# Kernel optimization log

Measured on AMD Instinct MI355X. Metric: run time of the kernel, lower is better.

## Reference

```python
import jax, jax.numpy as jnp
import numpy as np

# Config matching init_kwargs / input shapes
DIM = 96        # dim == C
NH = 6          # num_heads
KS = 7          # kernel_size (local window)
GW = 4          # group_width for the grouped conv in Hadamard-attn branch
B, D, H, W = 2, 8, 96, 96
HD = DIM // NH          # head dim (dim_qk == dim_v == dim)
SCALE = HD ** -0.5      # qk_scale default: head_dim**-0.5
PAD = KS // 2
EPS = 1e-5


def setup_inputs() -> dict:
    key = jax.random.key(0)
    ks = jax.random.split(key, 10)
    s = 0.02
    return {
        "x": jax.random.normal(ks[0], (B, DIM, D, H, W), jnp.float32),
        # pre-norm LayerNorm params
        "ln_g": jnp.ones((DIM,), jnp.float32),
        "ln_b": jnp.zeros((DIM,), jnp.float32),
        # q,k projection (fused 1x1): out = 2*dim_qk
        "w_qk": s * jax.random.normal(ks[1], (2 * DIM, DIM), jnp.float32),
        "b_qk": jnp.zeros((2 * DIM,), jnp.float32),
        # v projection (1x1)
        "w_v": s * jax.random.normal(ks[2], (DIM, DIM), jnp.float32),
        "b_v": jnp.zeros((DIM,), jnp.float32),
        # Hadamard-attention branch: grouped KSxKS conv (groups = DIM//GW)
        "w_a1": s * jax.random.normal(ks[3], (DIM, GW, KS, KS), jnp.float32),
        "b_a1": jnp.zeros((DIM,), jnp.float32),
        # 1x1 conv producing per-head local attention logits (NH * KS^2 channels)
        "w_a2": s * jax.random.normal(ks[4], (NH * KS * KS, DIM), jnp.float32),
        "b_a2": jnp.zeros((NH * KS * KS,), jnp.float32),
        # ghost head (lam=1, gamma=1): attn = h_attn * ghost_mul + ghost_add
        "g_mul": 1.0 + s * jax.random.normal(ks[5], (NH * KS * KS,), jnp.float32),
        "g_add": s * jax.random.normal(ks[6], (NH * KS * KS,), jnp.float32),
        # output projection (1x1)
        "w_p": s * jax.random.normal(ks[7], (DIM, DIM), jnp.float32),
        "b_p": jnp.zeros((DIM,), jnp.float32),
    }


def _elsa_block(x, ln_g, ln_b, w_qk, b_qk, w_v, b_v, w_a1, b_a1, w_a2, b_a2,
                g_mul, g_add, w_p, b_p):
    """x: (Bp, H, W, C) channel-last frames. Pre-norm residual ELSA attention."""
    Bp, Hh, Ww, C = x.shape
    # LayerNorm over channels
    mu = jnp.mean(x, axis=-1, keepdims=True)
    var = jnp.mean(jnp.square(x - mu), axis=-1, keepdims=True)
    xn = (x - mu) * jax.lax.rsqrt(var + EPS) * ln_g + ln_b

    # 1x1 q,k,v projections (channel-last matmuls)
    qk = xn @ w_qk.T + b_qk                      # (Bp,H,W,2C)
    q, k = jnp.split(qk, 2, axis=-1)
    v = xn @ w_v.T + b_v                         # (Bp,H,W,C)

    # Hadamard product -> attention logits via grouped conv + GELU + 1x1
    h = jnp.transpose(q * k * SCALE, (0, 3, 1, 2))   # (Bp,C,H,W) NCHW
    a = jax.lax.conv_general_dilated(
        h, w_a1, window_strides=(1, 1), padding='SAME',
        feature_group_count=C // GW) + b_a1[None, :, None, None]
    a = jax.nn.gelu(a, approximate=False)
    a = jnp.einsum('bchw,oc->bohw', a, w_a2) + b_a2[None, :, None, None]

    # ghost head (lam=1, gamma=1): elementwise scale + static bias per (head, tap)
    attn = a * g_mul[None, :, None, None] + g_add[None, :, None, None]
    attn = attn.reshape(Bp, NH, KS * KS, Hh, Ww)     # (Bp,nh,k^2,H,W)

    # local window aggregation (unfold-free: 49 shifted fused multiply-adds)
    vr = jnp.transpose(v, (0, 3, 1, 2)).reshape(Bp, NH, HD, Hh, Ww)
    vp = jnp.pad(vr, ((0, 0), (0, 0), (0, 0), (PAD, PAD), (PAD, PAD)))
    out = jnp.zeros_like(vr)
    for i in range(KS):
        for j in range(KS):
            out = out + attn[:, :, i * KS + j, None] * vp[:, :, :, i:i + Hh, j:j + Ww]

    out = jnp.transpose(out.reshape(Bp, C, Hh, Ww), (0, 2, 3, 1))  # (Bp,H,W,C)
    y = out @ w_p.T + b_p
    return x + y


def reference(x, ln_g, ln_b, w_qk, b_qk, w_v, b_v, w_a1, b_a1, w_a2, b_a2,
              g_mul, g_add, w_p, b_p):
    b, c, d, hh, ww = x.shape
    # 'b c s h w -> (b s) h w c'
    xf = jnp.transpose(x, (0, 2, 3, 4, 1)).reshape(b * d, hh, ww, c)
    yf = _elsa_block(xf, ln_g, ln_b, w_qk, b_qk, w_v, b_v, w_a1, b_a1,
                     w_a2, b_a2, g_mul, g_add, w_p, b_p)
    # '(b s) h w c -> b c s h w'
    return jnp.transpose(yf.reshape(b, d, hh, ww, c), (0, 4, 1, 2, 3))
```

## Files before the change

### kernel.cpp

```cpp
#include <hip/hip_runtime.h>
#include <hip/hip_bf16.h>


typedef unsigned short u16;
typedef short bf16x8 __attribute__((ext_vector_type(8)));
typedef float floatx4 __attribute__((ext_vector_type(4)));
typedef unsigned short ushort8 __attribute__((ext_vector_type(8)));
typedef unsigned short ushort4v __attribute__((ext_vector_type(4)));
typedef unsigned int uint4v __attribute__((ext_vector_type(4)));
typedef unsigned int uint2v __attribute__((ext_vector_type(2)));

#define PIX      9216
#define SCALE_QK 0.25f

__device__ __forceinline__ float b2f(u16 u) {
  union { unsigned int i; float f; } z; z.i = ((unsigned int)u) << 16; return z.f;
}
__device__ __forceinline__ float lo2f(unsigned int u) {
  union { unsigned int i; float f; } z; z.i = u << 16; return z.f;
}
__device__ __forceinline__ float hi2f(unsigned int u) {
  union { unsigned int i; float f; } z; z.i = u & 0xFFFF0000u; return z.f;
}
__device__ __forceinline__ u16 f2b(float f) {
  union { float f; unsigned int i; } z; z.f = f;
  unsigned int r = z.i + 0x7fffu + ((z.i >> 16) & 1u);
  return (u16)(r >> 16);
}

__global__ void k_prep(const float* __restrict__ w_qk, const float* __restrict__ b_qk,
                       const float* __restrict__ w_v,  const float* __restrict__ b_v,
                       const float* __restrict__ w_a1,
                       const float* __restrict__ w_a2, const float* __restrict__ b_a2,
                       const float* __restrict__ g_mul,const float* __restrict__ g_add,
                       const float* __restrict__ w_p,  const float* __restrict__ b_p,
                       u16* __restrict__ W2, float* __restrict__ bias2,
                       u16* __restrict__ WA2, float* __restrict__ biasA2,
                       u16* __restrict__ WP, float* __restrict__ biasP,
                       float* __restrict__ WC1) {
  int i = blockIdx.x * 256 + threadIdx.x;
  if (i < 30720) {
    int r = i / 96, ci = i % 96;
    float val = 0.f;
    if (r < 192) { int src = (r & 1) ? (96 + (r >> 1)) : (r >> 1); val = w_qk[src * 96 + ci]; }
    else if (r < 288) val = w_v[(r - 192) * 96 + ci];
    W2[i] = f2b(val);
  } else if (i < 31040) {
    int r = i - 30720; float bv = 0.f;
    if (r < 192) { int src = (r & 1) ? (96 + (r >> 1)) : (r >> 1); bv = b_qk[src]; }
    else if (r < 288) bv = b_v[r - 192];
    bias2[r] = bv;
  } else if (i < 61760) {
    int j = i - 31040; int r = j / 96, ci = j % 96;
    float wv = 0.f;
    if (r < 294) wv = w_a2[r * 96 + ci] * g_mul[r];
    WA2[j] = f2b(wv);
  } else if (i < 62080) {
    int r = i - 61760; float bv = 0.f;
    if (r < 294) bv = b_a2[r] * g_mul[r] + g_add[r];
    biasA2[r] = bv;
  } else if (i < 74368) {
    int j = i - 62080; int r = j / 96;
    WP[j] = (r < 96) ? f2b(w_p[j]) : (u16)0;
  } else if (i < 74496) {
    int r = i - 74368;
    biasP[r] = (r < 96) ? b_p[r] : 0.f;
  } else if (i < 93312) {
    int j = i - 74496;
    int co = j & 3, kx = (j >> 2) % 7, ky = (j / 28) % 7, ch = (j / 196) & 3, g = j / 784;
    WC1[j] = w_a1[(g * 4 + co) * 196 + ch * 49 + ky * 7 + kx];
  }
}

__global__ __launch_bounds__(256) void k_ln(const float* __restrict__ x,
                                            const float* __restrict__ lg,
                                            const float* __restrict__ lb,
                                            u16* __restrict__ xn) {
  int idx = blockIdx.x * 256 + threadIdx.x;
  int f = idx / PIX, p = idx % PIX;
  int b = f >> 3, d = f & 7;
  size_t base = ((size_t)(b * 768 + d)) * PIX + p;
  float s = 0.f, ss = 0.f;
  for (int c = 0; c < 96; ++c) {
    float v = x[base + (size_t)c * 73728];
    s += v; ss += v * v;
  }
  float mu = s * (1.f / 96.f);
  float var = ss * (1.f / 96.f) - mu * mu;
  float rs = rsqrtf(var + 1e-5f);
  size_t ob = (size_t)idx * 96;
  for (int c0 = 0; c0 < 96; c0 += 8) {
    ushort8 pack;
    for (int u = 0; u < 8; ++u) {
      int c = c0 + u;
      float v = x[base + (size_t)c * 73728];
      pack[u] = f2b((v - mu) * rs * lg[c] + lb[c]);
    }
    *(ushort8*)&xn[ob + c0] = pack;
  }
}

template <int MODE>
__global__ __launch_bounds__(256) void k_gemm(const u16* __restrict__ X,
                                              const u16* __restrict__ W,
                                              const float* __restrict__ bias,
                                              u16* __restrict__ out0,
                                              u16* __restrict__ out1,
                                              float* __restrict__ outF,
                                              const float* __restrict__ resid,
                                              int fArg) {
  __shared__ u16 lw[64 * 104];
  __shared__ u16 lx[64 * 104];
  const int tid = threadIdx.x;
  const int fc = blockIdx.z;
  const int f = (MODE == 1) ? (fArg + fc) : fc;
  const int p0 = blockIdx.x * 64;
  const int cot = blockIdx.y;

  if constexpr (MODE == 0) {
    for (int ch = tid; ch < 768; ch += 256) {
      int r = ch / 12, s2 = ch % 12;
      *(uint4v*)&lw[r * 104 + s2 * 8] = *(const uint4v*)&W[(size_t)(cot * 64 + r) * 96 + s2 * 8];
      *(uint4v*)&lx[r * 104 + s2 * 8] = *(const uint4v*)&X[((size_t)(f * PIX + p0 + r)) * 96 + s2 * 8];
    }
  } else {
    for (int ch = tid; ch < 768; ch += 256) {
      int r = ch / 12, s2 = ch % 12;
      *(uint4v*)&lw[r * 104 + s2 * 8] = *(const uint4v*)&W[(size_t)(cot * 64 + r) * 96 + s2 * 8];
    }
    for (int idx = tid; idx < 768; idx += 256) {
      int s2 = idx >> 6, r = idx & 63;
      const u16* src0 = &X[((size_t)(f * 24 + 2 * s2) * PIX + p0 + r) * 4];
      const u16* src1 = &X[((size_t)(f * 24 + 2 * s2 + 1) * PIX + p0 + r) * 4];
      *(uint2v*)&lx[r * 104 + s2 * 8]     = *(const uint2v*)src0;
      *(uint2v*)&lx[r * 104 + s2 * 8 + 4] = *(const uint2v*)src1;
    }
  }
  __syncthreads();

  const int lane = tid & 63, wv = tid >> 6;
  const int cw = (wv >> 1) * 32, pw = (wv & 1) * 32;
  const int m = lane & 15, quad = lane >> 4;

  floatx4 acc[2][2] = {};
  for (int ks = 0; ks < 3; ++ks) {
    int ko = ks * 32 + quad * 8;
    bf16x8 a0 = *(const bf16x8*)&lw[(cw + m) * 104 + ko];
    bf16x8 a1 = *(const bf16x8*)&lw[(cw + 16 + m) * 104 + ko];
    bf16x8 b0 = *(const bf16x8*)&lx[(pw + m) * 104 + ko];
    bf16x8 b1 = *(const bf16x8*)&lx[(pw + 16 + m) * 104 + ko];
    acc[0][0] = __builtin_amdgcn_mfma_f32_16x16x32_bf16(a0, b0, acc[0][0], 0, 0, 0);
    acc[0][1] = __builtin_amdgcn_mfma_f32_16x16x32_bf16(a0, b1, acc[0][1], 0, 0, 0);
    acc[1][0] = __builtin_amdgcn_mfma_f32_16x16x32_bf16(a1, b0, acc[1][0], 0, 0, 0);
    acc[1][1] = __builtin_amdgcn_mfma_f32_16x16x32_bf16(a1, b1, acc[1][1], 0, 0, 0);
  }

  for (int mt = 0; mt < 2; ++mt)
    for (int nt = 0; nt < 2; ++nt) {
      int R = cot * 64 + cw + mt * 16 + quad * 4;
      int pc = p0 + pw + nt * 16 + m;
      floatx4 v4 = acc[mt][nt];
      if (MODE == 0) {
        if (cot < 3) {
          float q0 = v4[0] + bias[R + 0], k0 = v4[1] + bias[R + 1];
          float q1 = v4[2] + bias[R + 2], k1 = v4[3] + bias[R + 3];
          int hc = R >> 1;
          out0[((size_t)f * 96 + hc) * PIX + pc]     = f2b(q0 * k0 * SCALE_QK);
          out0[((size_t)f * 96 + hc + 1) * PIX + pc] = f2b(q1 * k1 * SCALE_QK);
        } else {
          for (int r = 0; r < 4; ++r) {
            int vr = R + r - 192;
            if (vr < 96) out1[((size_t)f * 96 + vr) * PIX + pc] = f2b(v4[r] + bias[R + r]);
          }
        }
      } else if (MODE == 1) {
        for (int r = 0; r < 4; ++r) {
          int o = R + r;
          if (o < 294) out0[((size_t)fc * 294 + o) * PIX + pc] = f2b(v4[r] + bias[o]);
        }
      } else {
        int b = f >> 3, d = f & 7;
        for (int r = 0; r < 4; ++r) {
          int o = R + r;
          if (o < 96) {
            size_t gi = ((size_t)(b * 96 + o) * 8 + d) * PIX + pc;
            outF[gi] = resid[gi] + v4[r] + bias[o];
          }
        }
      }
    }
}

__global__ __launch_bounds__(256, 4) void k_conv(const u16* __restrict__ h,
                                                 const float* __restrict__ wc1,
                                                 const float* __restrict__ b_a1,
                                                 u16* __restrict__ a_t) {
  __shared__ u16 li[4 * 22 * 104];
  const int g = blockIdx.x, ty = blockIdx.y, f = blockIdx.z;
  const int tid = threadIdx.x;
  const int gb = g * 4, y0 = ty * 16;
  for (int idx = tid; idx < 4 * 22 * 104; idx += 256) {
    int col = idx % 104;
    int rr = (idx / 104) % 22;
    int ch = idx / (104 * 22);
    int ax = col - 3, ay = y0 - 3 + rr;
    u16 v = 0;
    if (ax >= 0 && ax < 96 && ay >= 0 && ay < 96)
      v = h[((size_t)f * 96 + gb + ch) * PIX + ay * 96 + ax];
    li[idx] = v;
  }
  __syncthreads();

  const int y = tid >> 4;
  const int x0 = (tid & 15) * 6;
  float acc[4][6];
  #pragma unroll
  for (int co = 0; co < 4; ++co) {
    float bv = b_a1[gb + co];
    #pragma unroll
    for (int o = 0; o < 6; ++o) acc[co][o] = bv;
  }

  for (int ch = 0; ch < 4; ++ch)
    for (int ky = 0; ky < 7; ++ky) {
      const float* wrow = &wc1[(((g * 4 + ch) * 7) + ky) * 28];
      float w[28];
      #pragma unroll
      for (int t = 0; t < 28; ++t) w[t] = wrow[t];
      const unsigned int* lsrc =
          (const unsigned int*)&li[(ch * 22 + (y + ky)) * 104 + x0];
      float in[12];
      #pragma unroll
      for (int t = 0; t < 6; ++t) {
        unsigned int u = lsrc[t];
        in[2 * t]     = lo2f(u);
        in[2 * t + 1] = hi2f(u);
      }
      #pragma unroll
      for (int kx = 0; kx < 7; ++kx)
        #pragma unroll
        for (int o = 0; o < 6; ++o)
          #pragma unroll
          for (int co = 0; co < 4; ++co)
            acc[co][o] += w[kx * 4 + co] * in[o + kx];
    }

  size_t obase = ((size_t)(f * 24 + g) * PIX + (size_t)(y0 + y) * 96 + x0) * 4;
  #pragma unroll
  for (int o = 0; o < 6; o += 2) {
    ushort8 r8;
    #pragma unroll
    for (int co = 0; co < 4; ++co) {
      float a0 = acc[co][o], a1 = acc[co][o + 1];
      r8[co]     = f2b(0.5f * a0 * (1.f + erff(a0 * 0.70710678118f)));
      r8[co + 4] = f2b(0.5f * a1 * (1.f + erff(a1 * 0.70710678118f)));
    }
    *(ushort8*)&a_t[obase + o * 4] = r8;
  }
}

__global__ __launch_bounds__(256, 4) void k_aggr(const u16* __restrict__ attn_c,
                                                 const u16* __restrict__ v,
                                                 u16* __restrict__ out_t,
                                                 int fbase) {
  __shared__ u16 lv[4 * 22 * 104];
  const int wgid = blockIdx.x + 24 * (blockIdx.y + 6 * blockIdx.z);
  const int xcd = wgid & 7;
  const int member = (wgid >> 3) & 3;
  const int slot = wgid >> 5;
  const int gidx = slot * 8 + xcd;
  const int cqh = gidx % 6;
  const int ty = (gidx / 6) % 6;
  const int fc = gidx / 36;
  const int cq = cqh * 4 + member;
  const int f = fbase + fc;
  const int tid = threadIdx.x;
  const int c0 = cq * 4, y0 = ty * 16;
  const int head = c0 >> 4;
  for (int idx = tid; idx < 4 * 22 * 104; idx += 256) {
    int col = idx % 104;
    int rr = (idx / 104) % 22;
    int ch = idx / (104 * 22);
    int ax = col - 3, ay = y0 - 3 + rr;
    u16 val = 0;
    if (ax >= 0 && ax < 96 && ay >= 0 && ay < 96)
      val = v[((size_t)f * 96 + c0 + ch) * PIX + ay * 96 + ax];
    lv[idx] = val;
  }
  __syncthreads();

  const int y = tid >> 4;
  const int x0 = (tid & 15) * 6;
  float acc[4][6] = {};
  const int prow = (y0 + y) * 96 + x0;

  for (int i = 0; i < 7; ++i) {
    float vrow[4][12];
    #pragma unroll
    for (int ch = 0; ch < 4; ++ch) {
      const unsigned int* lsrc = (const unsigned int*)&lv[(ch * 22 + (y + i)) * 104 + x0];
      #pragma unroll
      for (int t = 0; t < 6; ++t) {
        unsigned int u = lsrc[t];
        vrow[ch][2 * t]     = lo2f(u);
        vrow[ch][2 * t + 1] = hi2f(u);
      }
    }
    #pragma unroll
    for (int j = 0; j < 7; ++j) {
      const unsigned int* asrc = (const unsigned int*)
          &attn_c[((size_t)fc * 294 + head * 49 + i * 7 + j) * PIX + prow];
      unsigned int u0 = asrc[0], u1 = asrc[1], u2 = asrc[2];
      float av[6] = {lo2f(u0), hi2f(u0), lo2f(u1), hi2f(u1), lo2f(u2), hi2f(u2)};
      #pragma unroll
      for (int o = 0; o < 6; ++o)
        #pragma unroll
        for (int ch = 0; ch < 4; ++ch)
          acc[ch][o] += av[o] * vrow[ch][o + j];
    }
  }

  size_t obase = ((size_t)(f * 24 + cq) * PIX + prow) * 4;
  #pragma unroll
  for (int o = 0; o < 6; o += 2) {
    ushort8 r8;
    #pragma unroll
    for (int ch = 0; ch < 4; ++ch) {
      r8[ch]     = f2b(acc[ch][o]);
      r8[ch + 4] = f2b(acc[ch][o + 1]);
    }
    *(ushort8*)&out_t[obase + o * 4] = r8;
  }
}

extern "C" void kernel_launch(void* const* d_in, const int* in_sizes, int n_in,
                              void* d_out, int out_size, void* d_ws, size_t ws_size,
                              hipStream_t stream) {
  const float* x    = (const float*)d_in[0];
  const float* ln_g = (const float*)d_in[1];
  const float* ln_b = (const float*)d_in[2];
  const float* w_qk = (const float*)d_in[3];
  const float* b_qk = (const float*)d_in[4];
  const float* w_v  = (const float*)d_in[5];
  const float* b_v  = (const float*)d_in[6];
  const float* w_a1 = (const float*)d_in[7];
  const float* b_a1 = (const float*)d_in[8];
  const float* w_a2 = (const float*)d_in[9];
  const float* b_a2 = (const float*)d_in[10];
  const float* g_mul= (const float*)d_in[11];
  const float* g_add= (const float*)d_in[12];
  const float* w_p  = (const float*)d_in[13];
  const float* b_p  = (const float*)d_in[14];

  char* ws = (char*)d_ws;
  u16*   W2    = (u16*)(ws + 0);
  float* bias2 = (float*)(ws + 61440);
  u16*   WA2   = (u16*)(ws + 62720);
  float* biasA2= (float*)(ws + 124160);
  u16*   WP    = (u16*)(ws + 125440);
  float* biasP = (float*)(ws + 150016);
  float* WC1   = (float*)(ws + 150528);
  u16*   xn_t  = (u16*)(ws + 225792);
  u16*   hbuf  = (u16*)(ws + 28537344);
  u16*   vbuf  = (u16*)(ws + 56848896);
  u16*   attnc = (u16*)(ws + 85160448);

  k_prep<<<365, 256, 0, stream>>>(w_qk, b_qk, w_v, b_v, w_a1, w_a2, b_a2, g_mul, g_add,
                                  w_p, b_p, W2, bias2, WA2, biasA2, WP, biasP, WC1);
  k_ln<<<576, 256, 0, stream>>>(x, ln_g, ln_b, xn_t);
  k_gemm<0><<<dim3(144, 5, 16), 256, 0, stream>>>(xn_t, W2, bias2, hbuf, vbuf,
                                                  nullptr, nullptr, 0);
  k_conv<<<dim3(24, 6, 16), 256, 0, stream>>>(hbuf, WC1, b_a1, xn_t );
  for (int c = 0; c < 2; ++c) {
    k_gemm<1><<<dim3(144, 5, 8), 256, 0, stream>>>(xn_t , WA2, biasA2,
                                                   attnc, nullptr, nullptr, nullptr, c * 8);
    k_aggr<<<dim3(24, 6, 8), 256, 0, stream>>>(attnc, vbuf, hbuf , c * 8);
  }
  k_gemm<2><<<dim3(144, 2, 16), 256, 0, stream>>>(hbuf , WP, biasP,
                                                  nullptr, nullptr, (float*)d_out, x, 0);
}
```

Baseline: 408.3 us.

## Use packed fp16 dot2 in grouped conv and store Hadamard output as fp16

The Hadamard product q*k is now stored as fp16 instead of bf16. The grouped 7x7 conv now reads it as packed half pairs and accumulates with v_dot2 fp16 instructions. Weights are pre-packed into even/odd-aligned half pairs so each output needs four dot2 ops per row instead of seven scalar FMAs. The shared-memory fill is widened to 32-bit loads. This cuts ALU and LDS work in the conv but narrows dynamic range, since fp16 can overflow or lose small values where bf16 would not.

New measurement: 395.0 us. -3.2%, faster.

```diff
diff --git a/kernel.cpp b/kernel.cpp
--- a/kernel.cpp
+++ b/kernel.cpp
@@ -9,13 +9,11 @@
 typedef unsigned short ushort4v __attribute__((ext_vector_type(4)));
 typedef unsigned int uint4v __attribute__((ext_vector_type(4)));
 typedef unsigned int uint2v __attribute__((ext_vector_type(2)));
+typedef _Float16 f16x2 __attribute__((ext_vector_type(2)));
 
 #define PIX      9216
 #define SCALE_QK 0.25f
 
-__device__ __forceinline__ float b2f(u16 u) {
-  union { unsigned int i; float f; } z; z.i = ((unsigned int)u) << 16; return z.f;
-}
 __device__ __forceinline__ float lo2f(unsigned int u) {
   union { unsigned int i; float f; } z; z.i = u << 16; return z.f;
 }
@@ -26,6 +24,21 @@
   union { float f; unsigned int i; } z; z.f = f;
   unsigned int r = z.i + 0x7fffu + ((z.i >> 16) & 1u);
   return (u16)(r >> 16);
+}
+__device__ __forceinline__ u16 f2h(float f) {
+  _Float16 h = (_Float16)f;
+  union { _Float16 h; u16 u; } z; z.h = h; return z.u;
+}
+__device__ __forceinline__ f16x2 u2h(unsigned int u) {
+  union { unsigned int u; f16x2 h; } z; z.u = u; return z.h;
+}
+__device__ __forceinline__ float dot2(unsigned int w, unsigned int x, float acc) {
+#if __has_builtin(__builtin_amdgcn_fdot2)
+  return __builtin_amdgcn_fdot2(u2h(w), u2h(x), acc, false);
+#else
+  f16x2 a = u2h(w), b = u2h(x);
+  return acc + (float)a[0] * (float)b[0] + (float)a[1] * (float)b[1];
+#endif
 }
 
 __global__ void k_prep(const float* __restrict__ w_qk, const float* __restrict__ b_qk,
@@ -37,7 +50,7 @@
                        u16* __restrict__ W2, float* __restrict__ bias2,
                        u16* __restrict__ WA2, float* __restrict__ biasA2,
                        u16* __restrict__ WP, float* __restrict__ biasP,
-                       float* __restrict__ WC1) {
+                       unsigned int* __restrict__ WCV) {
   int i = blockIdx.x * 256 + threadIdx.x;
   if (i < 30720) {
     int r = i / 96, ci = i % 96;
@@ -67,8 +80,13 @@
     biasP[r] = (r < 96) ? b_p[r] : 0.f;
   } else if (i < 93312) {
     int j = i - 74496;
-    int co = j & 3, kx = (j >> 2) % 7, ky = (j / 28) % 7, ch = (j / 196) & 3, g = j / 784;
-    WC1[j] = w_a1[(g * 4 + co) * 196 + ch * 49 + ky * 7 + kx];
+    int u = j % 7, co = (j / 7) & 3, ky = (j / 28) % 7, ch = (j / 196) & 3, g = j / 784;
+    const float* wsrc = &w_a1[(g * 4 + co) * 196 + ch * 49 + ky * 7];
+    float a, b;
+    if (u < 3)       { a = wsrc[2 * u];     b = wsrc[2 * u + 1]; }
+    else if (u == 3) { a = wsrc[6];         b = 0.f; }
+    else             { int t = u - 3;       a = wsrc[2 * t - 1]; b = wsrc[2 * t]; }
+    WCV[j] = (unsigned int)f2h(a) | ((unsigned int)f2h(b) << 16);
   }
 }
 
@@ -165,8 +183,8 @@
           float q0 = v4[0] + bias[R + 0], k0 = v4[1] + bias[R + 1];
           float q1 = v4[2] + bias[R + 2], k1 = v4[3] + bias[R + 3];
           int hc = R >> 1;
-          out0[((size_t)f * 96 + hc) * PIX + pc]     = f2b(q0 * k0 * SCALE_QK);
-          out0[((size_t)f * 96 + hc + 1) * PIX + pc] = f2b(q1 * k1 * SCALE_QK);
+          out0[((size_t)f * 96 + hc) * PIX + pc]     = f2h(q0 * k0 * SCALE_QK);
+          out0[((size_t)f * 96 + hc + 1) * PIX + pc] = f2h(q1 * k1 * SCALE_QK);
         } else {
           for (int r = 0; r < 4; ++r) {
             int vr = R + r - 192;
@@ -192,22 +210,23 @@
 }
 
 __global__ __launch_bounds__(256, 4) void k_conv(const u16* __restrict__ h,
-                                                 const float* __restrict__ wc1,
+                                                 const unsigned int* __restrict__ wcv,
                                                  const float* __restrict__ b_a1,
                                                  u16* __restrict__ a_t) {
   __shared__ u16 li[4 * 22 * 104];
   const int g = blockIdx.x, ty = blockIdx.y, f = blockIdx.z;
   const int tid = threadIdx.x;
   const int gb = g * 4, y0 = ty * 16;
-  for (int idx = tid; idx < 4 * 22 * 104; idx += 256) {
-    int col = idx % 104;
-    int rr = (idx / 104) % 22;
-    int ch = idx / (104 * 22);
-    int ax = col - 3, ay = y0 - 3 + rr;
-    u16 v = 0;
-    if (ax >= 0 && ax < 96 && ay >= 0 && ay < 96)
-      v = h[((size_t)f * 96 + gb + ch) * PIX + ay * 96 + ax];
-    li[idx] = v;
+  for (int idx = tid; idx < 4576; idx += 256) {
+    int row = idx / 52;
+    int jd  = idx - row * 52;
+    int ch  = row / 22;
+    int rr  = row - ch * 22;
+    int ay  = y0 - 3 + rr;
+    unsigned int val = 0;
+    if (jd >= 2 && jd <= 49 && ay >= 0 && ay < 96)
+      val = *(const unsigned int*)&h[((size_t)f * 96 + gb + ch) * PIX + ay * 96 + (2 * jd - 4)];
+    *(unsigned int*)&li[row * 104 + 2 * jd] = val;
   }
   __syncthreads();
 
@@ -223,26 +242,33 @@
 
   for (int ch = 0; ch < 4; ++ch)
     for (int ky = 0; ky < 7; ++ky) {
-      const float* wrow = &wc1[(((g * 4 + ch) * 7) + ky) * 28];
-      float w[28];
-      #pragma unroll
-      for (int t = 0; t < 28; ++t) w[t] = wrow[t];
+      const unsigned int* wrow = &wcv[(((g * 4 + ch) * 7) + ky) * 28];
       const unsigned int* lsrc =
           (const unsigned int*)&li[(ch * 22 + (y + ky)) * 104 + x0];
-      float in[12];
+      unsigned int IN[7];
       #pragma unroll
-      for (int t = 0; t < 6; ++t) {
-        unsigned int u = lsrc[t];
-        in[2 * t]     = lo2f(u);
-        in[2 * t + 1] = hi2f(u);
+      for (int t = 0; t < 7; ++t) IN[t] = lsrc[t];
+      #pragma unroll
+      for (int co = 0; co < 4; ++co) {
+        unsigned int w0 = wrow[co * 7 + 0], w1 = wrow[co * 7 + 1];
+        unsigned int w2 = wrow[co * 7 + 2], w3 = wrow[co * 7 + 3];
+        unsigned int w4 = wrow[co * 7 + 4], w5 = wrow[co * 7 + 5];
+        unsigned int w6 = wrow[co * 7 + 6];
+        unsigned int o0 = w0 << 16;
+        float a;
+        a = acc[co][0]; a = dot2(o0, IN[0], a); a = dot2(w4, IN[1], a);
+                        a = dot2(w5, IN[2], a); a = dot2(w6, IN[3], a); acc[co][0] = a;
+        a = acc[co][1]; a = dot2(w0, IN[1], a); a = dot2(w1, IN[2], a);
+                        a = dot2(w2, IN[3], a); a = dot2(w3, IN[4], a); acc[co][1] = a;
+        a = acc[co][2]; a = dot2(o0, IN[1], a); a = dot2(w4, IN[2], a);
+                        a = dot2(w5, IN[3], a); a = dot2(w6, IN[4], a); acc[co][2] = a;
+        a = acc[co][3]; a = dot2(w0, IN[2], a); a = dot2(w1, IN[3], a);
+                        a = dot2(w2, IN[4], a); a = dot2(w3, IN[5], a); acc[co][3] = a;
+        a = acc[co][4]; a = dot2(o0, IN[2], a); a = dot2(w4, IN[3], a);
+                        a = dot2(w5, IN[4], a); a = dot2(w6, IN[5], a); acc[co][4] = a;
+        a = acc[co][5]; a = dot2(w0, IN[3], a); a = dot2(w1, IN[4], a);
+                        a = dot2(w2, IN[5], a); a = dot2(w3, IN[6], a); acc[co][5] = a;
       }
-      #pragma unroll
-      for (int kx = 0; kx < 7; ++kx)
-        #pragma unroll
-        for (int o = 0; o < 6; ++o)
-          #pragma unroll
-          for (int co = 0; co < 4; ++co)
-            acc[co][o] += w[kx * 4 + co] * in[o + kx];
     }
 
   size_t obase = ((size_t)(f * 24 + g) * PIX + (size_t)(y0 + y) * 96 + x0) * 4;
@@ -359,18 +385,18 @@
   float* biasA2= (float*)(ws + 124160);
   u16*   WP    = (u16*)(ws + 125440);
   float* biasP = (float*)(ws + 150016);
-  float* WC1   = (float*)(ws + 150528);
+  unsigned int* WCV = (unsigned int*)(ws + 150528);
   u16*   xn_t  = (u16*)(ws + 225792);
   u16*   hbuf  = (u16*)(ws + 28537344);
   u16*   vbuf  = (u16*)(ws + 56848896);
   u16*   attnc = (u16*)(ws + 85160448);
 
   k_prep<<<365, 256, 0, stream>>>(w_qk, b_qk, w_v, b_v, w_a1, w_a2, b_a2, g_mul, g_add,
-                                  w_p, b_p, W2, bias2, WA2, biasA2, WP, biasP, WC1);
+                                  w_p, b_p, W2, bias2, WA2, biasA2, WP, biasP, WCV);
   k_ln<<<576, 256, 0, stream>>>(x, ln_g, ln_b, xn_t);
   k_gemm<0><<<dim3(144, 5, 16), 256, 0, stream>>>(xn_t, W2, bias2, hbuf, vbuf,
                                                   nullptr, nullptr, 0);
-  k_conv<<<dim3(24, 6, 16), 256, 0, stream>>>(hbuf, WC1, b_a1, xn_t );
+  k_conv<<<dim3(24, 6, 16), 256, 0, stream>>>(hbuf, WCV, b_a1, xn_t );
   for (int c = 0; c < 2; ++c) {
     k_gemm<1><<<dim3(144, 5, 8), 256, 0, stream>>>(xn_t , WA2, biasA2,
                                                    attnc, nullptr, nullptr, nullptr, c * 8);
```
